# Kernel tuning notes

Measured on AMD Instinct MI355X. Metric: run time of the kernel, lower is better.

## Reference

```python
import jax, jax.numpy as jnp
import numpy as np

D_MODEL = 768
N_HEADS = 12
D_HEAD = D_MODEL // N_HEADS
TEMP = float(np.sqrt(D_HEAD))


def setup_inputs() -> dict:
    key = jax.random.key(0)
    ks = jax.random.split(key, 12)
    B, S, D = 8, 2048, D_MODEL
    patches = jax.random.normal(ks[0], (B, S, D), dtype=jnp.float32)
    in_weight = jax.random.uniform(ks[1], (D * 3, D), dtype=jnp.float32)
    in_bias = jax.random.uniform(ks[2], (D * 3,), dtype=jnp.float32)
    out_w = jax.random.normal(ks[3], (D, D), dtype=jnp.float32) * (1.0 / np.sqrt(D))
    out_b = jnp.zeros((D,), dtype=jnp.float32)
    mlp_w1 = jax.random.normal(ks[4], (4 * D, D), dtype=jnp.float32) * (1.0 / np.sqrt(D))
    mlp_b1 = jnp.zeros((4 * D,), dtype=jnp.float32)
    mlp_w2 = jax.random.normal(ks[5], (D, 4 * D), dtype=jnp.float32) * (1.0 / np.sqrt(4 * D))
    mlp_b2 = jnp.zeros((D,), dtype=jnp.float32)
    ln1_g = jnp.ones((D,), dtype=jnp.float32)
    ln1_b = jnp.zeros((D,), dtype=jnp.float32)
    ln2_g = jnp.ones((D,), dtype=jnp.float32)
    ln2_b = jnp.zeros((D,), dtype=jnp.float32)
    return {
        "patches": patches,
        "in_weight": in_weight, "in_bias": in_bias,
        "out_w": out_w, "out_b": out_b,
        "mlp_w1": mlp_w1, "mlp_b1": mlp_b1,
        "mlp_w2": mlp_w2, "mlp_b2": mlp_b2,
        "ln1_g": ln1_g, "ln1_b": ln1_b,
        "ln2_g": ln2_g, "ln2_b": ln2_b,
    }


def layer_norm(x, g, b, eps=1e-5):
    mu = jnp.mean(x, axis=-1, keepdims=True)
    var = jnp.var(x, axis=-1, keepdims=True)
    return (x - mu) * jax.lax.rsqrt(var + eps) * g + b


def mha(x, in_weight, in_bias, out_w, out_b):
    # Replicate quirky per-head reshape: [3D, D] -> [H, d_head, 3, D]
    W = in_weight.reshape(N_HEADS, D_HEAD, 3, D_MODEL)  # h, e, 3, d
    Bv = in_bias.reshape(N_HEADS, D_HEAD, 3)            # h, e, 3
    qw, kw, vw = W[:, :, 0, :], W[:, :, 1, :], W[:, :, 2, :]  # [H, e, D]
    qb, kb, vb = Bv[:, :, 0], Bv[:, :, 1], Bv[:, :, 2]        # [H, e]
    # Q,K,V per head: [B, H, S, e]
    Q = jnp.einsum('bsd,hed->bhse', x, qw) + qb[None, :, None, :]
    K = jnp.einsum('bsd,hed->bhse', x, kw) + kb[None, :, None, :]
    V = jnp.einsum('bsd,hed->bhse', x, vw) + vb[None, :, None, :]
    atn = jnp.einsum('bhse,bhte->bhst', Q, K)
    atn = jax.nn.softmax(atn / TEMP, axis=-1)
    # NOTE: original uses V (not atn @ V) as head output; heads concatenated over feature dim
    B_, H, S, e = V.shape
    heads = jnp.transpose(V, (0, 2, 1, 3)).reshape(B_, S, H * e)
    masks = jnp.sum(atn, axis=1)  # sum over heads: [B, S, S]
    out = heads @ out_w.T + out_b
    return out, masks


def reference(patches, in_weight, in_bias, out_w, out_b,
              mlp_w1, mlp_b1, mlp_w2, mlp_b2,
              ln1_g, ln1_b, ln2_g, ln2_b):
    x = layer_norm(patches, ln1_g, ln1_b)
    sa, _ = mha(x, in_weight, in_bias, out_w, out_b)
    x = sa + x  # dropout = identity (eval)
    x = layer_norm(x, ln2_g, ln2_b)
    h = jax.nn.selu(x @ mlp_w1.T + mlp_b1)
    x = (h @ mlp_w2.T + mlp_b2) + x
    return x
```

## Files before the change

### kernel.cpp

```cpp
#include <hip/hip_runtime.h>


typedef __bf16 bf16;
typedef __bf16 bf16x8 __attribute__((ext_vector_type(8)));
typedef __bf16 bf16x4 __attribute__((ext_vector_type(4)));
typedef float  f32x4  __attribute__((ext_vector_type(4)));

#define N_ROWS  16384

#define AS1(p) ((const __attribute__((address_space(1))) void*)(p))
#define AS3(p) ((__attribute__((address_space(3))) void*)(p))

#define VM4 0x0F74
#define VM0 0x0F70

#define N1 589824
#define N2 589824
#define N3 147456
__global__ __launch_bounds__(256) void prep_cast(const float* __restrict__ w1,
                                                 const float* __restrict__ w2,
                                                 const float* __restrict__ ow,
                                                 bf16* __restrict__ w1b,
                                                 bf16* __restrict__ w2b,
                                                 bf16* __restrict__ owb) {
  int i = blockIdx.x * 256 + threadIdx.x;
  const float* src; bf16* dst; int off;
  if (i < N1)           { src = w1; dst = w1b; off = i; }
  else if (i < N1 + N2) { src = w2; dst = w2b; off = i - N1; }
  else                  { src = ow; dst = owb; off = i - N1 - N2; }
  float4 v = ((const float4*)src)[off];
  bf16x4 o = {(bf16)v.x, (bf16)v.y, (bf16)v.z, (bf16)v.w};
  *(bf16x4*)(dst + 4 * (size_t)off) = o;
}

__global__ __launch_bounds__(256) void wvt_kernel(const float* __restrict__ in_weight,
                                                  bf16* __restrict__ wvt) {
  __shared__ float t[64][65];
  const int k0 = blockIdx.x * 64, j0 = blockIdx.y * 64;
  const int tx = threadIdx.x & 63, ty = threadIdx.x >> 6;
  for (int jj = ty; jj < 64; jj += 4)
    t[jj][tx] = in_weight[((size_t)(j0 + jj) * 3 + 2) * 768 + k0 + tx];
  __syncthreads();
  for (int kk = ty; kk < 64; kk += 4)
    wvt[(size_t)(k0 + kk) * 768 + j0 + tx] = (bf16)t[tx][kk];
}

__global__ __launch_bounds__(64) void bias_combine_kernel(const float* __restrict__ out_w,
                                                          const float* __restrict__ in_bias,
                                                          const float* __restrict__ out_b,
                                                          float* __restrict__ bc) {
  int n = blockIdx.x, l = threadIdx.x;
  float s = 0.f;
  for (int j = l; j < 768; j += 64) s += out_w[(size_t)n * 768 + j] * in_bias[j * 3 + 2];
#pragma unroll
  for (int off = 32; off > 0; off >>= 1) s += __shfl_xor(s, off, 64);
  if (l == 0) bc[n] = s + out_b[n];
}

template <typename TIN>
__global__ __launch_bounds__(256) void ln_kernel(const TIN* __restrict__ x,
                                                 const float* __restrict__ g,
                                                 const float* __restrict__ b,
                                                 bf16* __restrict__ y) {
  const int row = blockIdx.x;
  const TIN* xr = x + (size_t)row * 768;
  float v[3], s1 = 0.f, s2 = 0.f;
#pragma unroll
  for (int i = 0; i < 3; ++i) {
    v[i] = (float)xr[threadIdx.x + i * 256];
    s1 += v[i];
    s2 += v[i] * v[i];
  }
#pragma unroll
  for (int off = 32; off > 0; off >>= 1) {
    s1 += __shfl_xor(s1, off, 64);
    s2 += __shfl_xor(s2, off, 64);
  }
  __shared__ float red[8];
  int w = threadIdx.x >> 6, l = threadIdx.x & 63;
  if (l == 0) { red[w * 2] = s1; red[w * 2 + 1] = s2; }
  __syncthreads();
  s1 = red[0] + red[2] + red[4] + red[6];
  s2 = red[1] + red[3] + red[5] + red[7];
  const float mu = s1 * (1.f / 768.f);
  const float var = s2 * (1.f / 768.f) - mu * mu;
  const float rstd = rsqrtf(var + 1e-5f);
#pragma unroll
  for (int i = 0; i < 3; ++i) {
    int d = threadIdx.x + i * 256;
    y[(size_t)row * 768 + d] = (bf16)((v[i] - mu) * rstd * g[d] + b[d]);
  }
}

template <int EPI>
__global__ __launch_bounds__(512, 2) void gemm_bt(const bf16* __restrict__ A,
                                                  const bf16* __restrict__ B,
                                                  const float* __restrict__ bias,
                                                  const bf16* __restrict__ resid,
                                                  void* __restrict__ out,
                                                  int M, int N, int K) {
  __shared__ bf16 ring[65536];
  const int tid = threadIdx.x;
  const int w = tid >> 6, l = tid & 63;
  const int wr = w >> 2, wcn = w & 3;
  const int q = l >> 4, m16 = l & 15;

  int mtile, ntile;
  {
    const int L = blockIdx.y * gridDim.x + blockIdx.x;
    const int gy = gridDim.y;
    if ((gy & 7) == 0) {
      const int mpx = gy >> 3;
      const int xcd = L & 7;
      const int slot = L >> 3;
      mtile = xcd * mpx + (slot % mpx);
      ntile = slot / mpx;
    } else {
      mtile = blockIdx.y; ntile = blockIdx.x;
    }
  }
  const long tileM = (long)mtile * 256;
  const long tileN = (long)ntile * 256;

  const bf16* gA[2][2]; const bf16* gB[2][2];
  int lA[2][2], lB[2][2];
  {
    const int sc = l & 3;
#pragma unroll
    for (int j = 0; j < 2; ++j) {
      const int b = w * 2 + j;
      const int p = b >> 3, s = (b >> 2) & 1, blk = b & 3;
#pragma unroll
      for (int mh = 0; mh < 2; ++mh) {
        const int row = s * 128 + mh * 64 + blk * 16 + (l >> 2);
        const int cl = (sc - (row >> 1)) & 3;
        gA[mh][j] = A + (tileM + row) * (long)K + p * 32 + cl * 8;
        lA[mh][j] = p * 8192 + row * 32 + sc * 8;
      }
      const int rowB = b * 16 + (l >> 2);
      const int clB = (sc - (rowB >> 1)) & 3;
#pragma unroll
      for (int ks = 0; ks < 2; ++ks) {
        gB[ks][j] = B + (tileN + rowB) * (long)K + ks * 32 + clB * 8;
        lB[ks][j] = 16384 + ks * 8192 + rowB * 32 + sc * 8;
      }
    }
  }

  int offA[8], offB[4];
#pragma unroll
  for (int mh = 0; mh < 2; ++mh)
#pragma unroll
    for (int mi = 0; mi < 4; ++mi) {
      const int r = wr * 128 + mh * 64 + mi * 16 + m16;
      offA[mh * 4 + mi] = r * 32 + (((q + (r >> 1)) & 3) << 3);
    }
#pragma unroll
  for (int ni = 0; ni < 4; ++ni) {
    const int r = wcn * 64 + ni * 16 + m16;
    offB[ni] = r * 32 + (((q + (r >> 1)) & 3) << 3);
  }

  f32x4 acc[8][4] = {};

#define ST(GP, LO, BUF)                                                        \
  { bf16* bb = ring + (BUF) * 32768;                                           \
    __builtin_amdgcn_global_load_lds(AS1(GP[0]), AS3(bb + LO[0]), 16, 0, 0);   \
    __builtin_amdgcn_global_load_lds(AS1(GP[1]), AS3(bb + LO[1]), 16, 0, 0);   \
    GP[0] += 64; GP[1] += 64; }

  ST(gA[0], lA[0], 0) ST(gB[0], lB[0], 0) ST(gA[1], lA[1], 0) ST(gB[1], lB[1], 0)
  ST(gA[0], lA[0], 1) ST(gB[0], lB[0], 1)
  __builtin_amdgcn_s_waitcnt(VM4);
  __builtin_amdgcn_s_barrier();

#define PHASE(BUF, MH, KS, STG, DOVM, VMW)                                     \
  {                                                                            \
    const bf16* pa = ring + (BUF) * 32768 + (KS) * 8192;                       \
    const bf16* pb = ring + (BUF) * 32768 + 16384 + (KS) * 8192;               \
    bf16x8 af[4], bv[4];                                                       \
    _Pragma("unroll")                                                          \
    for (int mi = 0; mi < 4; ++mi)                                             \
      af[mi] = *(const bf16x8*)&pa[offA[(MH) * 4 + mi]];                       \
    _Pragma("unroll")                                                          \
    for (int ni = 0; ni < 4; ++ni)                                             \
      bv[ni] = *(const bf16x8*)&pb[offB[ni]];                                  \
    STG;                                                                       \
    if (DOVM) __builtin_amdgcn_s_waitcnt(VMW);                                 \
    __builtin_amdgcn_s_barrier();                                              \
    asm volatile("s_waitcnt lgkmcnt(0)");                                      \
    __builtin_amdgcn_s_setprio(1);                                             \
    _Pragma("unroll")                                                          \
    for (int mi = 0; mi < 4; ++mi) {                                           \
      _Pragma("unroll")                                                        \
      for (int ni = 0; ni < 4; ++ni)                                           \
        acc[(MH) * 4 + mi][ni] = __builtin_amdgcn_mfma_f32_16x16x32_bf16(      \
            af[mi], bv[ni], acc[(MH) * 4 + mi][ni], 0, 0, 0);                  \
    }                                                                          \
    __builtin_amdgcn_s_setprio(0);                                             \
    __builtin_amdgcn_s_barrier();                                              \
  }

  const int T = K >> 6;
#pragma unroll 1
  for (int i = 0; i < T / 2 - 1; ++i) {
    PHASE(0, 0, 0, ST(gA[1], lA[1], 1), 0, VM0)
    PHASE(0, 0, 1, ST(gB[1], lB[1], 1), 0, VM0)
    PHASE(0, 1, 0, ST(gA[0], lA[0], 0), 0, VM0)
    PHASE(0, 1, 1, ST(gB[0], lB[0], 0), 1, VM4)
    PHASE(1, 0, 0, ST(gA[1], lA[1], 0), 0, VM0)
    PHASE(1, 0, 1, ST(gB[1], lB[1], 0), 0, VM0)
    PHASE(1, 1, 0, ST(gA[0], lA[0], 1), 0, VM0)
    PHASE(1, 1, 1, ST(gB[0], lB[0], 1), 1, VM4)
  }
  PHASE(0, 0, 0, ST(gA[1], lA[1], 1), 0, VM0)
  PHASE(0, 0, 1, ST(gB[1], lB[1], 1), 0, VM0)
  PHASE(0, 1, 0, (void)0, 0, VM0)
  PHASE(0, 1, 1, (void)0, 1, VM0)
  PHASE(1, 0, 0, (void)0, 0, VM0)
  PHASE(1, 0, 1, (void)0, 0, VM0)
  PHASE(1, 1, 0, (void)0, 0, VM0)
  PHASE(1, 1, 1, (void)0, 0, VM0)
#undef PHASE
#undef ST

  const long colBase = tileN + (long)wcn * 64 + m16;
  const long rowBase = tileM + (long)wr * 128 + q * 4;
#pragma unroll
  for (int mi = 0; mi < 8; ++mi) {
#pragma unroll
    for (int r = 0; r < 4; ++r) {
      const long row = rowBase + mi * 16 + r;
#pragma unroll
      for (int ni = 0; ni < 4; ++ni) {
        const long col = colBase + ni * 16;
        float v = acc[mi][ni][r];
        if (EPI == 0) {
          ((bf16*)out)[row * N + col] = (bf16)v;
        } else if (EPI == 1) {
          v += bias[col] + (float)resid[row * N + col];
          ((float*)out)[row * N + col] = v;
        } else if (EPI == 2) {
          v += bias[col];
          v = v > 0.f ? 1.0507009873554805f * v
                      : 1.0507009873554805f * 1.6732632423543772f * (__expf(v) - 1.f);
          ((bf16*)out)[row * N + col] = (bf16)v;
        } else {
          v += bias[col] + (float)resid[row * N + col];
          ((bf16*)out)[row * N + col] = (bf16)v;
        }
      }
    }
  }
}

extern "C" void kernel_launch(void* const* d_in, const int* in_sizes, int n_in,
                              void* d_out, int out_size, void* d_ws, size_t ws_size,
                              hipStream_t stream) {
  const float* patches   = (const float*)d_in[0];
  const float* in_weight = (const float*)d_in[1];
  const float* in_bias   = (const float*)d_in[2];
  const float* out_w     = (const float*)d_in[3];
  const float* out_b     = (const float*)d_in[4];
  const float* mlp_w1    = (const float*)d_in[5];
  const float* mlp_b1    = (const float*)d_in[6];
  const float* mlp_w2    = (const float*)d_in[7];
  const float* mlp_b2    = (const float*)d_in[8];
  const float* ln1_g     = (const float*)d_in[9];
  const float* ln1_b     = (const float*)d_in[10];
  const float* ln2_g     = (const float*)d_in[11];
  const float* ln2_b     = (const float*)d_in[12];

  char* ws = (char*)d_ws;
  const size_t MB = 1024 * 1024;
  bf16* Wc   = (bf16*)(ws + 0);
  bf16* w1b  = (bf16*)(ws + 2 * MB);
  bf16* w2b  = (bf16*)(ws + 8 * MB);
  bf16* owb  = (bf16*)(ws + 14 * MB);
  bf16* wvt  = (bf16*)(ws + 16 * MB);
  float* bc  = (float*)(ws + 18 * MB);
  bf16* X1   = (bf16*)(ws + 20 * MB);
  bf16* X3   = (bf16*)(ws + 20 * MB);
  bf16* X2b  = (bf16*)(ws + 48 * MB);
  bf16* H    = (bf16*)(ws + 48 * MB);

  prep_cast<<<(N1 + N2 + N3) / 256, 256, 0, stream>>>(mlp_w1, mlp_w2, out_w,
                                                      w1b, w2b, owb);
  wvt_kernel<<<dim3(12, 12), 256, 0, stream>>>(in_weight, wvt);
  bias_combine_kernel<<<768, 64, 0, stream>>>(out_w, in_bias, out_b, bc);
  gemm_bt<0><<<dim3(3, 3), 512, 0, stream>>>(owb, wvt, nullptr, nullptr, Wc, 768, 768, 768);

  ln_kernel<float><<<N_ROWS, 256, 0, stream>>>(patches, ln1_g, ln1_b, X1);
  gemm_bt<3><<<dim3(3, 64), 512, 0, stream>>>(X1, Wc, bc, X1, X2b, N_ROWS, 768, 768);
  ln_kernel<bf16><<<N_ROWS, 256, 0, stream>>>(X2b, ln2_g, ln2_b, X3);
  gemm_bt<2><<<dim3(12, 64), 512, 0, stream>>>(X3, w1b, mlp_b1, nullptr, H, N_ROWS, 3072, 768);
  gemm_bt<1><<<dim3(3, 64), 512, 0, stream>>>(H, w2b, mlp_b2, X3, d_out, N_ROWS, 768, 3072);
}
```

Measured before the change: 396.6 us.

## Reorder GEMM phases to reuse B fragments and retune load-wait schedule

Reorders the eight MFMA phases per iteration in a serpentine pattern so that consecutive phases share the same B sub-tile. The B fragment registers are then loaded from LDS only every other phase, halving B LDS reads. The global-to-LDS staging order and the vmcnt wait thresholds are reworked to match, and pointer increments are replaced by per-slot K offsets. This aims to cut LDS read traffic and latency per phase, at the cost of a more intricate and fragile buffer-readiness schedule.

```diff
diff --git a/kernel.cpp b/kernel.cpp
--- a/kernel.cpp
+++ b/kernel.cpp
@@ -11,8 +11,11 @@
 #define AS1(p) ((const __attribute__((address_space(1))) void*)(p))
 #define AS3(p) ((__attribute__((address_space(3))) void*)(p))
 
-#define VM4 0x0F74
-#define VM0 0x0F70
+#define WAIT8  __builtin_amdgcn_s_waitcnt(0x0F78)
+#define WAIT6  __builtin_amdgcn_s_waitcnt(0x0F76)
+#define WAIT2  __builtin_amdgcn_s_waitcnt(0x0F72)
+#define WAIT0  __builtin_amdgcn_s_waitcnt(0x0F70)
+#define NOWAIT (void)0
 
 #define N1 589824
 #define N2 589824
@@ -163,30 +166,37 @@
 
   f32x4 acc[8][4] = {};
 
-#define ST(GP, LO, BUF)                                                        \
+  int kb0A0 = 0, kb0B0 = 0, kb0B1 = 0, kb0A1 = 0;
+  int kb1A0 = 64, kb1B0 = 64, kb1B1 = 64, kb1A1 = 64;
+
+#define ST(BP, LO, BUF, KV)                                                    \
   { bf16* bb = ring + (BUF) * 32768;                                           \
-    __builtin_amdgcn_global_load_lds(AS1(GP[0]), AS3(bb + LO[0]), 16, 0, 0);   \
-    __builtin_amdgcn_global_load_lds(AS1(GP[1]), AS3(bb + LO[1]), 16, 0, 0);   \
-    GP[0] += 64; GP[1] += 64; }
-
-  ST(gA[0], lA[0], 0) ST(gB[0], lB[0], 0) ST(gA[1], lA[1], 0) ST(gB[1], lB[1], 0)
-  ST(gA[0], lA[0], 1) ST(gB[0], lB[0], 1)
-  __builtin_amdgcn_s_waitcnt(VM4);
+    __builtin_amdgcn_global_load_lds(AS1((BP)[0] + (KV)), AS3(bb + (LO)[0]), 16, 0, 0); \
+    __builtin_amdgcn_global_load_lds(AS1((BP)[1] + (KV)), AS3(bb + (LO)[1]), 16, 0, 0); \
+    (KV) += 128; }
+
+  ST(gA[0], lA[0], 0, kb0A0) ST(gB[0], lB[0], 0, kb0B0)
+  ST(gA[1], lA[1], 0, kb0A1) ST(gB[1], lB[1], 0, kb0B1)
+  ST(gB[1], lB[1], 1, kb1B1) ST(gA[1], lA[1], 1, kb1A1)
+  WAIT6;
   __builtin_amdgcn_s_barrier();
 
-#define PHASE(BUF, MH, KS, STG, DOVM, VMW)                                     \
+  bf16x8 bv[4];
+#define PHASE(BUF, MH, KS, LB, STG, WSTMT)                                     \
   {                                                                            \
     const bf16* pa = ring + (BUF) * 32768 + (KS) * 8192;                       \
     const bf16* pb = ring + (BUF) * 32768 + 16384 + (KS) * 8192;               \
-    bf16x8 af[4], bv[4];                                                       \
+    bf16x8 af[4];                                                              \
     _Pragma("unroll")                                                          \
     for (int mi = 0; mi < 4; ++mi)                                             \
       af[mi] = *(const bf16x8*)&pa[offA[(MH) * 4 + mi]];                       \
-    _Pragma("unroll")                                                          \
-    for (int ni = 0; ni < 4; ++ni)                                             \
-      bv[ni] = *(const bf16x8*)&pb[offB[ni]];                                  \
+    if (LB) {                                                                  \
+      _Pragma("unroll")                                                        \
+      for (int ni = 0; ni < 4; ++ni)                                           \
+        bv[ni] = *(const bf16x8*)&pb[offB[ni]];                                \
+    }                                                                          \
     STG;                                                                       \
-    if (DOVM) __builtin_amdgcn_s_waitcnt(VMW);                                 \
+    WSTMT;                                                                     \
     __builtin_amdgcn_s_barrier();                                              \
     asm volatile("s_waitcnt lgkmcnt(0)");                                      \
     __builtin_amdgcn_s_setprio(1);                                             \
@@ -204,23 +214,23 @@
   const int T = K >> 6;
 #pragma unroll 1
   for (int i = 0; i < T / 2 - 1; ++i) {
-    PHASE(0, 0, 0, ST(gA[1], lA[1], 1), 0, VM0)
-    PHASE(0, 0, 1, ST(gB[1], lB[1], 1), 0, VM0)
-    PHASE(0, 1, 0, ST(gA[0], lA[0], 0), 0, VM0)
-    PHASE(0, 1, 1, ST(gB[0], lB[0], 0), 1, VM4)
-    PHASE(1, 0, 0, ST(gA[1], lA[1], 0), 0, VM0)
-    PHASE(1, 0, 1, ST(gB[1], lB[1], 0), 0, VM0)
-    PHASE(1, 1, 0, ST(gA[0], lA[0], 1), 0, VM0)
-    PHASE(1, 1, 1, ST(gB[0], lB[0], 1), 1, VM4)
-  }
-  PHASE(0, 0, 0, ST(gA[1], lA[1], 1), 0, VM0)
-  PHASE(0, 0, 1, ST(gB[1], lB[1], 1), 0, VM0)
-  PHASE(0, 1, 0, (void)0, 0, VM0)
-  PHASE(0, 1, 1, (void)0, 1, VM0)
-  PHASE(1, 0, 0, (void)0, 0, VM0)
-  PHASE(1, 0, 1, (void)0, 0, VM0)
-  PHASE(1, 1, 0, (void)0, 0, VM0)
-  PHASE(1, 1, 1, (void)0, 0, VM0)
+    PHASE(0, 0, 0, 1, ST(gA[0], lA[0], 1, kb1A0), NOWAIT)
+    PHASE(0, 1, 0, 0, ST(gB[0], lB[0], 1, kb1B0), WAIT8)
+    PHASE(0, 1, 1, 1, ST(gB[0], lB[0], 0, kb0B0), NOWAIT)
+    PHASE(0, 0, 1, 0, ST(gA[1], lA[1], 0, kb0A1), WAIT6)
+    PHASE(1, 0, 1, 1, ST(gA[0], lA[0], 0, kb0A0), NOWAIT)
+    PHASE(1, 1, 1, 0, ST(gB[1], lB[1], 0, kb0B1), WAIT8)
+    PHASE(1, 1, 0, 1, ST(gB[1], lB[1], 1, kb1B1), NOWAIT)
+    PHASE(1, 0, 0, 0, ST(gA[1], lA[1], 1, kb1A1), WAIT6)
+  }
+  PHASE(0, 0, 0, 1, ST(gA[0], lA[0], 1, kb1A0), NOWAIT)
+  PHASE(0, 1, 0, 0, ST(gB[0], lB[0], 1, kb1B0), WAIT8)
+  PHASE(0, 1, 1, 1, (void)0, NOWAIT)
+  PHASE(0, 0, 1, 0, (void)0, WAIT2)
+  PHASE(1, 0, 1, 1, (void)0, NOWAIT)
+  PHASE(1, 1, 1, 0, (void)0, WAIT0)
+  PHASE(1, 1, 0, 1, (void)0, NOWAIT)
+  PHASE(1, 0, 0, 0, (void)0, NOWAIT)
 #undef PHASE
 #undef ST
 
```

Result: no change. 390.1 us (-1.7%).
